# Optimization experiments

Hardware: AMD Instinct MI355X
Metric: run time of the kernel (lower is better)

## Reference

```python
import jax, jax.numpy as jnp
import numpy as np

NUM_EMBEDDINGS = 1024
EMBEDDING_DIM = 64
BETA = 0.25  # commitment_cost


def setup_inputs() -> dict:
    key = jax.random.key(0)
    k1, k2 = jax.random.split(key)
    z = jax.random.normal(k1, (32, EMBEDDING_DIM, 32, 32), dtype=jnp.float32)
    embedding = jax.random.normal(k2, (NUM_EMBEDDINGS, EMBEDDING_DIM), dtype=jnp.float32)
    return {"z": z, "embedding": embedding}


def reference(z, embedding):
    B, D, H, W = z.shape
    beta = jnp.asarray(BETA, z.dtype)
    # [B, D, H, W] -> [B*H*W, D]
    z_flat = jnp.transpose(z, (0, 2, 3, 1)).reshape(-1, D)
    # squared L2 distances to each code: ||z||^2 - 2 z.e^T + ||e||^2  -> [N, E]
    dist = (
        jnp.sum(z_flat * z_flat, axis=1, keepdims=True)
        - 2.0 * (z_flat @ embedding.T)
        + jnp.sum(embedding * embedding, axis=1)
    )
    encoding_indices = jnp.argmin(dist, axis=1)  # [N]
    # direct gather instead of one-hot matmul (same math)
    quantized = embedding[encoding_indices]  # [N, D]
    quantized = jnp.transpose(quantized.reshape(B, H, W, D), (0, 3, 1, 2))
    commitment_loss = beta * jnp.mean(
        (jax.lax.stop_gradient(z) - quantized) ** 2
    )
    codebook_loss = jnp.mean((z - jax.lax.stop_gradient(quantized)) ** 2)
    loss = commitment_loss + codebook_loss
    # straight-through estimator
    quantized_st = z + jax.lax.stop_gradient(quantized - z)
    return (quantized_st, loss, encoding_indices)
```

## Files before the change

kernel.cpp:

```cpp
#include <hip/hip_runtime.h>

typedef __attribute__((ext_vector_type(8))) short short8;
typedef __attribute__((ext_vector_type(4))) float f32x4;
typedef unsigned int uint32;

#define QOUT 2097152

__device__ __forceinline__ unsigned short f2bf(float f){
  uint32 u = __float_as_uint(f);
  return (unsigned short)((u + 0x7FFFu + ((u >> 16) & 1u)) >> 16);
}
__device__ __forceinline__ float bf2f(unsigned short h){
  return __uint_as_float(((uint32)h) << 16);
}
__device__ __forceinline__ uint32 med3u(uint32 a, uint32 b, uint32 c){
  uint32 d;
  asm("v_med3_u32 %0, %1, %2, %3" : "=v"(d) : "v"(a), "v"(b), "v"(c));
  return d;
}
__device__ __forceinline__ void glds16(const unsigned char* g, unsigned char* l){
  __builtin_amdgcn_global_load_lds(
      (const __attribute__((address_space(1))) unsigned int*)g,
      (__attribute__((address_space(3))) unsigned int*)l, 16, 0, 0);
}

__global__ void vq_prep(const float* __restrict__ emb, unsigned char* __restrict__ ebg,
                        float* __restrict__ nrm64, int* __restrict__ cnt){
  int gt = blockIdx.x * 256 + threadIdx.x;
  if (gt == 0) *cnt = 0;
  int C = gt >> 4, sub = gt & 15;
  float4 v = reinterpret_cast<const float4*>(emb)[C * 16 + sub];
  float s = v.x*v.x + v.y*v.y + v.z*v.z + v.w*v.w;
  ushort4 h, l;
  h.x = f2bf(v.x); l.x = f2bf(v.x - bf2f(h.x));
  h.y = f2bf(v.y); l.y = f2bf(v.y - bf2f(h.y));
  h.z = f2bf(v.z); l.z = f2bf(v.z - bf2f(h.z));
  h.w = f2bf(v.w); l.w = f2bf(v.w - bf2f(h.w));
  int cc = C & 127;
  int off = (C >> 7) * 32768 + cc * 128 + ((sub ^ ((cc & 7) << 1)) << 3);
  *reinterpret_cast<ushort4*>(ebg + off) = h;
  *reinterpret_cast<ushort4*>(ebg + 16384 + off) = l;
#pragma unroll
  for (int d = 1; d < 16; d <<= 1) s += __shfl_xor(s, d);
  if (sub == 0) nrm64[C] = 0.5f * s + 128.0f;
}

__global__ __launch_bounds__(256, 2) void vq_main(
    const float* __restrict__ z, const float* __restrict__ emb,
    const unsigned char* __restrict__ ebg, const float* __restrict__ nrm64,
    float* __restrict__ out, float* __restrict__ partial, int* __restrict__ cnt)
{
  __shared__ __align__(16) unsigned char LB[65536];
  __shared__ float nrmlds[1024];
  __shared__ uint32 mg[64][2][3];
  __shared__ uint32 cand[64][4];
  __shared__ int kidx[64];
  __shared__ float werr[4];
  __shared__ float red[256];
  __shared__ int isLast;

  const int t = threadIdx.x;
  const int bi = blockIdx.x;
  const int n0 = bi * 64;
  const int b = n0 >> 10;
  const int hw0 = n0 & 1023;
  const int w = t >> 6, lane = t & 63;
  const int wm = w >> 1, wn = w & 1;
  const int l15 = lane & 15, g = lane >> 4;

  for (int i = t; i < 1024; i += 256) nrmlds[i] = nrm64[i];

  float* zf = reinterpret_cast<float*>(LB + 32768);
#pragma unroll
  for (int k = 0; k < 16; ++k){
    int li = k * 256 + t;
    int d = li >> 6, j = li & 63;
    zf[j * 68 + d] = z[((b * 64 + d) << 10) + hw0 + j];
  }
  __syncthreads();

#pragma unroll
  for (int r = 0; r < 8; ++r){
    int off = (r * 4 + w) * 1024;
    glds16(ebg + off + lane * 16, LB + off);
  }

  short8 ah[2][2], al[2][2];
#pragma unroll
  for (int mf = 0; mf < 2; ++mf)
#pragma unroll
    for (int kf = 0; kf < 2; ++kf){
      int row = wm * 32 + mf * 16 + l15;
      int base = row * 68 + kf * 32 + g * 8;
      float4 q0 = *reinterpret_cast<float4*>(&zf[base]);
      float4 q1 = *reinterpret_cast<float4*>(&zf[base + 4]);
      float vv[8] = {q0.x,q0.y,q0.z,q0.w,q1.x,q1.y,q1.z,q1.w};
#pragma unroll
      for (int j = 0; j < 8; ++j){
        float v = -vv[j];
        unsigned short hs = f2bf(v);
        unsigned short ls = f2bf(v - bf2f(hs));
        ah[mf][kf][j] = (short)hs;
        al[mf][kf][j] = (short)ls;
      }
    }
  __syncthreads();

  uint32 u0[8], u1[8], u2[8];
#pragma unroll
  for (int s = 0; s < 8; ++s){ u0[s] = 0xFFFFFFFFu; u1[s] = 0xFFFFFFFFu; u2[s] = 0xFFFFFFFFu; }

  const int cc0 = wn * 64 + l15;
  const int xsw = (l15 & 7) << 1;
  const int v0s = ((g * 2) ^ xsw) << 3;
  const int v1s = ((8 + g * 2) ^ xsw) << 3;

  for (int h = 0; h < 8; ++h){
    if (h < 7){
      const unsigned char* src = ebg + (h + 1) * 32768;
      unsigned char* dst = LB + (((h + 1) & 1) << 15);
#pragma unroll
      for (int r = 0; r < 8; ++r){
        int off = (r * 4 + w) * 1024;
        glds16(src + off + lane * 16, dst + off);
      }
    }
    const unsigned char* bufb = LB + ((h & 1) << 15);
#pragma unroll
    for (int nf = 0; nf < 4; ++nf){
      int cc = cc0 + nf * 16;
      const unsigned char* rb = bufb + cc * 128;
      short8 bh0 = *reinterpret_cast<const short8*>(rb + v0s);
      short8 bh1 = *reinterpret_cast<const short8*>(rb + v1s);
      short8 bl0 = *reinterpret_cast<const short8*>(rb + 16384 + v0s);
      short8 bl1 = *reinterpret_cast<const short8*>(rb + 16384 + v1s);
      int code = (h << 7) + cc;
      float nv = nrmlds[code];
      f32x4 a0 = {nv, nv, nv, nv};
      f32x4 a1 = {nv, nv, nv, nv};
      a0 = __builtin_amdgcn_mfma_f32_16x16x32_bf16(ah[0][0], bh0, a0, 0,0,0);
      a0 = __builtin_amdgcn_mfma_f32_16x16x32_bf16(ah[0][1], bh1, a0, 0,0,0);
      a0 = __builtin_amdgcn_mfma_f32_16x16x32_bf16(al[0][0], bh0, a0, 0,0,0);
      a0 = __builtin_amdgcn_mfma_f32_16x16x32_bf16(al[0][1], bh1, a0, 0,0,0);
      a0 = __builtin_amdgcn_mfma_f32_16x16x32_bf16(ah[0][0], bl0, a0, 0,0,0);
      a0 = __builtin_amdgcn_mfma_f32_16x16x32_bf16(ah[0][1], bl1, a0, 0,0,0);
      a1 = __builtin_amdgcn_mfma_f32_16x16x32_bf16(ah[1][0], bh0, a1, 0,0,0);
      a1 = __builtin_amdgcn_mfma_f32_16x16x32_bf16(ah[1][1], bh1, a1, 0,0,0);
      a1 = __builtin_amdgcn_mfma_f32_16x16x32_bf16(al[1][0], bh0, a1, 0,0,0);
      a1 = __builtin_amdgcn_mfma_f32_16x16x32_bf16(al[1][1], bh1, a1, 0,0,0);
      a1 = __builtin_amdgcn_mfma_f32_16x16x32_bf16(ah[1][0], bl0, a1, 0,0,0);
      a1 = __builtin_amdgcn_mfma_f32_16x16x32_bf16(ah[1][1], bl1, a1, 0,0,0);
      uint32 kb = (uint32)code;
#pragma unroll
      for (int r = 0; r < 4; ++r){
        uint32 k0v = (__float_as_uint(a0[r]) & 0xFFFFFC00u) | kb;
        u2[r] = med3u(k0v, u1[r], u2[r]);
        u1[r] = med3u(k0v, u0[r], u1[r]);
        u0[r] = u0[r] < k0v ? u0[r] : k0v;
        uint32 k1v = (__float_as_uint(a1[r]) & 0xFFFFFC00u) | kb;
        u2[4+r] = med3u(k1v, u1[4+r], u2[4+r]);
        u1[4+r] = med3u(k1v, u0[4+r], u1[4+r]);
        u0[4+r] = u0[4+r] < k1v ? u0[4+r] : k1v;
      }
    }
    __syncthreads();
  }

#pragma unroll
  for (int dm = 1; dm < 16; dm <<= 1){
#pragma unroll
    for (int s = 0; s < 8; ++s){
      uint32 x0 = (uint32)__shfl_xor((int)u0[s], dm);
      uint32 x1 = (uint32)__shfl_xor((int)u1[s], dm);
      uint32 x2 = (uint32)__shfl_xor((int)u2[s], dm);
      u2[s] = med3u(x0, u1[s], u2[s]); u1[s] = med3u(x0, u0[s], u1[s]); u0[s] = u0[s] < x0 ? u0[s] : x0;
      u2[s] = med3u(x1, u1[s], u2[s]); u1[s] = med3u(x1, u0[s], u1[s]); u0[s] = u0[s] < x1 ? u0[s] : x1;
      u2[s] = med3u(x2, u1[s], u2[s]); u1[s] = med3u(x2, u0[s], u1[s]); u0[s] = u0[s] < x2 ? u0[s] : x2;
    }
  }
  if (l15 == 0){
#pragma unroll
    for (int mf = 0; mf < 2; ++mf)
#pragma unroll
      for (int r = 0; r < 4; ++r){
        int lr = wm * 32 + mf * 16 + g * 4 + r;
        int s = mf * 4 + r;
        mg[lr][wn][0] = u0[s]; mg[lr][wn][1] = u1[s]; mg[lr][wn][2] = u2[s];
      }
  }
  __syncthreads();

  if (t < 64){
    uint32 a0k = mg[t][0][0], a1k = mg[t][0][1], a2k = mg[t][0][2];
#pragma unroll
    for (int j2 = 0; j2 < 3; ++j2){
      uint32 x = mg[t][1][j2];
      a2k = med3u(x, a1k, a2k); a1k = med3u(x, a0k, a1k); a0k = a0k < x ? a0k : x;
    }
    kidx[t] = (int)(a0k & 1023u);
    float d0 = __uint_as_float(a0k & 0xFFFFFC00u);
    float d1 = __uint_as_float(a1k & 0xFFFFFC00u);
    cand[t][0] = a0k; cand[t][1] = a1k; cand[t][2] = a2k;
    cand[t][3] = (d1 - d0 < 0.0625f) ? 1u : 0u;
  }
  __syncthreads();

  {
    int row = t >> 2, j = t & 3;
    if (cand[row][3]){
      double s = 1e300; int myk = 0x7FFFFFFF;
      if (j < 3){
        int k = (int)(cand[row][j] & 1023u);
        const float* zb = z + (b << 16) + hw0 + row;
        const float* e = emb + k * 64;
        double acc = 0.0;
        for (int d = 0; d < 64; ++d){
          double df = (double)zb[d << 10] - (double)e[d];
          acc += df * df;
        }
        s = acc; myk = k;
      }
#pragma unroll
      for (int dx = 1; dx < 4; dx <<= 1){
        double so = __shfl_xor(s, dx);
        int ko = __shfl_xor(myk, dx);
        if (so < s || (so == s && ko < myk)) { s = so; myk = ko; }
      }
      if (j == 0) kidx[row] = myk;
    }
  }
  __syncthreads();

  {
    int row = t & 63, dp = t >> 6;
    int k = kidx[row];
    const float* e = emb + k * 64;
    const float* zb = z + (b << 16) + hw0 + row;
    float* ob = out + (b << 16) + hw0 + row;
    float err = 0.f;
#pragma unroll
    for (int dd = 0; dd < 16; ++dd){
      int d = dp * 16 + dd;
      float zv = zb[d << 10];
      float qv = e[d];
      ob[d << 10] = qv;
      float df = zv - qv;
      err = fmaf(df, df, err);
    }
    if (dp == 0) out[QOUT + 1 + n0 + row] = (float)k;
#pragma unroll
    for (int dx = 1; dx < 64; dx <<= 1) err += __shfl_xor(err, dx);
    if (lane == 0) werr[w] = err;
  }
  __syncthreads();
  if (t == 0){
    partial[bi] = (werr[0] + werr[1]) + (werr[2] + werr[3]);
    __threadfence();
    int pos = atomicAdd(cnt, 1);
    isLast = (pos == 511) ? 1 : 0;
  }
  __syncthreads();

  if (isLast){
    __threadfence();
    const volatile float* vp = partial;
    red[t] = vp[t] + vp[t + 256];
    __syncthreads();
    for (int ww = 128; ww > 0; ww >>= 1){
      if (t < ww) red[t] += red[t + ww];
      __syncthreads();
    }
    if (t == 0) out[QOUT] = 1.25f * red[0] * (1.0f / 2097152.0f);
  }
}

extern "C" void kernel_launch(void* const* d_in, const int* in_sizes, int n_in,
                              void* d_out, int out_size, void* d_ws, size_t ws_size,
                              hipStream_t stream) {
  const float* z   = (const float*)d_in[0];
  const float* emb = (const float*)d_in[1];
  float* out = (float*)d_out;
  unsigned char* ebg = (unsigned char*)d_ws;
  float* nrm64   = (float*)(ebg + 262144);
  float* partial = nrm64 + 1024;
  int*   cnt     = (int*)(partial + 512);

  vq_prep <<<64,  256, 0, stream>>>(emb, ebg, nrm64, cnt);
  vq_main <<<512, 256, 0, stream>>>(z, emb, ebg, nrm64, out, partial, cnt);
}
```

Baseline: 47.73 us.

## Stream codebook fragments directly from global memory instead of LDS double-buffering

The prep kernel now writes the bf16 hi/lo codebook in a fragment-ready layout, so each lane can load its MFMA B operands with 16-byte global (L2-cached) loads. The main kernel no longer stages the codebook in a 64KB double-buffered LDS ring and no longer needs the barriers of that ring. LDS drops to the z tile and small buffers, which may allow more resident blocks. The refine and output phases also reuse z from LDS rather than re-reading global memory. The risk is that per-iteration global load latency, with no explicit prefetch, is exposed in the MFMA loop.

New measurement: 42.88 us. 10.2% less time.

```diff
diff --git a/kernel.cpp b/kernel.cpp
--- a/kernel.cpp
+++ b/kernel.cpp
@@ -18,31 +18,32 @@
   asm("v_med3_u32 %0, %1, %2, %3" : "=v"(d) : "v"(a), "v"(b), "v"(c));
   return d;
 }
-__device__ __forceinline__ void glds16(const unsigned char* g, unsigned char* l){
-  __builtin_amdgcn_global_load_lds(
-      (const __attribute__((address_space(1))) unsigned int*)g,
-      (__attribute__((address_space(3))) unsigned int*)l, 16, 0, 0);
-}
 
 __global__ void vq_prep(const float* __restrict__ emb, unsigned char* __restrict__ ebg,
                         float* __restrict__ nrm64, int* __restrict__ cnt){
-  int gt = blockIdx.x * 256 + threadIdx.x;
-  if (gt == 0) *cnt = 0;
-  int C = gt >> 4, sub = gt & 15;
-  float4 v = reinterpret_cast<const float4*>(emb)[C * 16 + sub];
-  float s = v.x*v.x + v.y*v.y + v.z*v.z + v.w*v.w;
-  ushort4 h, l;
-  h.x = f2bf(v.x); l.x = f2bf(v.x - bf2f(h.x));
-  h.y = f2bf(v.y); l.y = f2bf(v.y - bf2f(h.y));
-  h.z = f2bf(v.z); l.z = f2bf(v.z - bf2f(h.z));
-  h.w = f2bf(v.w); l.w = f2bf(v.w - bf2f(h.w));
-  int cc = C & 127;
-  int off = (C >> 7) * 32768 + cc * 128 + ((sub ^ ((cc & 7) << 1)) << 3);
-  *reinterpret_cast<ushort4*>(ebg + off) = h;
-  *reinterpret_cast<ushort4*>(ebg + 16384 + off) = l;
-#pragma unroll
-  for (int d = 1; d < 16; d <<= 1) s += __shfl_xor(s, d);
-  if (sub == 0) nrm64[C] = 0.5f * s + 128.0f;
+  int u = blockIdx.x * 256 + threadIdx.x;
+  if (u == 0) *cnt = 0;
+  int C = u >> 3, oct = u & 7;
+  const float4* e4 = reinterpret_cast<const float4*>(emb) + C * 16 + oct * 2;
+  float4 v0 = e4[0], v1 = e4[1];
+  float vv[8] = {v0.x, v0.y, v0.z, v0.w, v1.x, v1.y, v1.z, v1.w};
+  float s = 0.f;
+  short8 H, L;
+#pragma unroll
+  for (int j = 0; j < 8; ++j){
+    float v = vv[j];
+    s = fmaf(v, v, s);
+    unsigned short hs = f2bf(v);
+    unsigned short ls = f2bf(v - bf2f(hs));
+    H[j] = (short)hs; L[j] = (short)ls;
+  }
+  int ng = C >> 4, c15 = C & 15, kf = oct >> 2, gg = oct & 3;
+  unsigned char* base = ebg + ng * 4096 + kf * 2048 + (gg * 16 + c15) * 16;
+  *reinterpret_cast<short8*>(base) = H;
+  *reinterpret_cast<short8*>(base + 1024) = L;
+#pragma unroll
+  for (int d = 1; d < 8; d <<= 1) s += __shfl_xor(s, d);
+  if (oct == 0) nrm64[C] = 0.5f * s + 128.0f;
 }
 
 __global__ __launch_bounds__(256, 2) void vq_main(
@@ -50,7 +51,7 @@
     const unsigned char* __restrict__ ebg, const float* __restrict__ nrm64,
     float* __restrict__ out, float* __restrict__ partial, int* __restrict__ cnt)
 {
-  __shared__ __align__(16) unsigned char LB[65536];
+  __shared__ float zf[64 * 68];
   __shared__ float nrmlds[1024];
   __shared__ uint32 mg[64][2][3];
   __shared__ uint32 cand[64][4];
@@ -68,9 +69,9 @@
   const int wm = w >> 1, wn = w & 1;
   const int l15 = lane & 15, g = lane >> 4;
 
-  for (int i = t; i < 1024; i += 256) nrmlds[i] = nrm64[i];
-
-  float* zf = reinterpret_cast<float*>(LB + 32768);
+#pragma unroll
+  for (int i = 0; i < 4; ++i) nrmlds[i * 256 + t] = nrm64[i * 256 + t];
+
 #pragma unroll
   for (int k = 0; k < 16; ++k){
     int li = k * 256 + t;
@@ -78,12 +79,6 @@
     zf[j * 68 + d] = z[((b * 64 + d) << 10) + hw0 + j];
   }
   __syncthreads();
-
-#pragma unroll
-  for (int r = 0; r < 8; ++r){
-    int off = (r * 4 + w) * 1024;
-    glds16(ebg + off + lane * 16, LB + off);
-  }
 
   short8 ah[2][2], al[2][2];
 #pragma unroll
@@ -104,66 +99,48 @@
         al[mf][kf][j] = (short)ls;
       }
     }
-  __syncthreads();
 
   uint32 u0[8], u1[8], u2[8];
 #pragma unroll
   for (int s = 0; s < 8; ++s){ u0[s] = 0xFFFFFFFFu; u1[s] = 0xFFFFFFFFu; u2[s] = 0xFFFFFFFFu; }
 
-  const int cc0 = wn * 64 + l15;
-  const int xsw = (l15 & 7) << 1;
-  const int v0s = ((g * 2) ^ xsw) << 3;
-  const int v1s = ((8 + g * 2) ^ xsw) << 3;
-
-  for (int h = 0; h < 8; ++h){
-    if (h < 7){
-      const unsigned char* src = ebg + (h + 1) * 32768;
-      unsigned char* dst = LB + (((h + 1) & 1) << 15);
-#pragma unroll
-      for (int r = 0; r < 8; ++r){
-        int off = (r * 4 + w) * 1024;
-        glds16(src + off + lane * 16, dst + off);
-      }
-    }
-    const unsigned char* bufb = LB + ((h & 1) << 15);
-#pragma unroll
-    for (int nf = 0; nf < 4; ++nf){
-      int cc = cc0 + nf * 16;
-      const unsigned char* rb = bufb + cc * 128;
-      short8 bh0 = *reinterpret_cast<const short8*>(rb + v0s);
-      short8 bh1 = *reinterpret_cast<const short8*>(rb + v1s);
-      short8 bl0 = *reinterpret_cast<const short8*>(rb + 16384 + v0s);
-      short8 bl1 = *reinterpret_cast<const short8*>(rb + 16384 + v1s);
-      int code = (h << 7) + cc;
-      float nv = nrmlds[code];
-      f32x4 a0 = {nv, nv, nv, nv};
-      f32x4 a1 = {nv, nv, nv, nv};
-      a0 = __builtin_amdgcn_mfma_f32_16x16x32_bf16(ah[0][0], bh0, a0, 0,0,0);
-      a0 = __builtin_amdgcn_mfma_f32_16x16x32_bf16(ah[0][1], bh1, a0, 0,0,0);
-      a0 = __builtin_amdgcn_mfma_f32_16x16x32_bf16(al[0][0], bh0, a0, 0,0,0);
-      a0 = __builtin_amdgcn_mfma_f32_16x16x32_bf16(al[0][1], bh1, a0, 0,0,0);
-      a0 = __builtin_amdgcn_mfma_f32_16x16x32_bf16(ah[0][0], bl0, a0, 0,0,0);
-      a0 = __builtin_amdgcn_mfma_f32_16x16x32_bf16(ah[0][1], bl1, a0, 0,0,0);
-      a1 = __builtin_amdgcn_mfma_f32_16x16x32_bf16(ah[1][0], bh0, a1, 0,0,0);
-      a1 = __builtin_amdgcn_mfma_f32_16x16x32_bf16(ah[1][1], bh1, a1, 0,0,0);
-      a1 = __builtin_amdgcn_mfma_f32_16x16x32_bf16(al[1][0], bh0, a1, 0,0,0);
-      a1 = __builtin_amdgcn_mfma_f32_16x16x32_bf16(al[1][1], bh1, a1, 0,0,0);
-      a1 = __builtin_amdgcn_mfma_f32_16x16x32_bf16(ah[1][0], bl0, a1, 0,0,0);
-      a1 = __builtin_amdgcn_mfma_f32_16x16x32_bf16(ah[1][1], bl1, a1, 0,0,0);
-      uint32 kb = (uint32)code;
-#pragma unroll
-      for (int r = 0; r < 4; ++r){
-        uint32 k0v = (__float_as_uint(a0[r]) & 0xFFFFFC00u) | kb;
-        u2[r] = med3u(k0v, u1[r], u2[r]);
-        u1[r] = med3u(k0v, u0[r], u1[r]);
-        u0[r] = u0[r] < k0v ? u0[r] : k0v;
-        uint32 k1v = (__float_as_uint(a1[r]) & 0xFFFFFC00u) | kb;
-        u2[4+r] = med3u(k1v, u1[4+r], u2[4+r]);
-        u1[4+r] = med3u(k1v, u0[4+r], u1[4+r]);
-        u0[4+r] = u0[4+r] < k1v ? u0[4+r] : k1v;
-      }
-    }
-    __syncthreads();
+  const unsigned char* pbase = ebg + (wn << 17) + (lane << 4);
+#pragma unroll
+  for (int i = 0; i < 32; ++i){
+    const unsigned char* p = pbase + (i << 12);
+    short8 bh0 = *reinterpret_cast<const short8*>(p);
+    short8 bl0 = *reinterpret_cast<const short8*>(p + 1024);
+    short8 bh1 = *reinterpret_cast<const short8*>(p + 2048);
+    short8 bl1 = *reinterpret_cast<const short8*>(p + 3072);
+    int ng = wn * 32 + i;
+    int code = (ng << 4) + l15;
+    float nv = nrmlds[code];
+    f32x4 a0 = {nv, nv, nv, nv};
+    f32x4 a1 = {nv, nv, nv, nv};
+    a0 = __builtin_amdgcn_mfma_f32_16x16x32_bf16(ah[0][0], bh0, a0, 0,0,0);
+    a0 = __builtin_amdgcn_mfma_f32_16x16x32_bf16(ah[0][1], bh1, a0, 0,0,0);
+    a0 = __builtin_amdgcn_mfma_f32_16x16x32_bf16(al[0][0], bh0, a0, 0,0,0);
+    a0 = __builtin_amdgcn_mfma_f32_16x16x32_bf16(al[0][1], bh1, a0, 0,0,0);
+    a0 = __builtin_amdgcn_mfma_f32_16x16x32_bf16(ah[0][0], bl0, a0, 0,0,0);
+    a0 = __builtin_amdgcn_mfma_f32_16x16x32_bf16(ah[0][1], bl1, a0, 0,0,0);
+    a1 = __builtin_amdgcn_mfma_f32_16x16x32_bf16(ah[1][0], bh0, a1, 0,0,0);
+    a1 = __builtin_amdgcn_mfma_f32_16x16x32_bf16(ah[1][1], bh1, a1, 0,0,0);
+    a1 = __builtin_amdgcn_mfma_f32_16x16x32_bf16(al[1][0], bh0, a1, 0,0,0);
+    a1 = __builtin_amdgcn_mfma_f32_16x16x32_bf16(al[1][1], bh1, a1, 0,0,0);
+    a1 = __builtin_amdgcn_mfma_f32_16x16x32_bf16(ah[1][0], bl0, a1, 0,0,0);
+    a1 = __builtin_amdgcn_mfma_f32_16x16x32_bf16(ah[1][1], bl1, a1, 0,0,0);
+    uint32 kb = (uint32)code;
+#pragma unroll
+    for (int r = 0; r < 4; ++r){
+      uint32 k0v = (__float_as_uint(a0[r]) & 0xFFFFFC00u) | kb;
+      u2[r] = med3u(k0v, u1[r], u2[r]);
+      u1[r] = med3u(k0v, u0[r], u1[r]);
+      u0[r] = u0[r] < k0v ? u0[r] : k0v;
+      uint32 k1v = (__float_as_uint(a1[r]) & 0xFFFFFC00u) | kb;
+      u2[4+r] = med3u(k1v, u1[4+r], u2[4+r]);
+      u1[4+r] = med3u(k1v, u0[4+r], u1[4+r]);
+      u0[4+r] = u0[4+r] < k1v ? u0[4+r] : k1v;
+    }
   }
 
 #pragma unroll
@@ -211,11 +188,10 @@
       double s = 1e300; int myk = 0x7FFFFFFF;
       if (j < 3){
         int k = (int)(cand[row][j] & 1023u);
-        const float* zb = z + (b << 16) + hw0 + row;
         const float* e = emb + k * 64;
         double acc = 0.0;
         for (int d = 0; d < 64; ++d){
-          double df = (double)zb[d << 10] - (double)e[d];
+          double df = (double)zf[row * 68 + d] - (double)e[d];
           acc += df * df;
         }
         s = acc; myk = k;
@@ -235,13 +211,12 @@
     int row = t & 63, dp = t >> 6;
     int k = kidx[row];
     const float* e = emb + k * 64;
-    const float* zb = z + (b << 16) + hw0 + row;
     float* ob = out + (b << 16) + hw0 + row;
     float err = 0.f;
 #pragma unroll
     for (int dd = 0; dd < 16; ++dd){
       int d = dp * 16 + dd;
-      float zv = zb[d << 10];
+      float zv = zf[row * 68 + d];
       float qv = e[d];
       ob[d << 10] = qv;
       float df = zv - qv;
@@ -285,6 +260,6 @@
   float* partial = nrm64 + 1024;
   int*   cnt     = (int*)(partial + 512);
 
-  vq_prep <<<64,  256, 0, stream>>>(emb, ebg, nrm64, cnt);
+  vq_prep <<<32,  256, 0, stream>>>(emb, ebg, nrm64, cnt);
   vq_main <<<512, 256, 0, stream>>>(z, emb, ebg, nrm64, out, partial, cnt);
 }
```
